# Kernel optimization log

Hardware: AMD Instinct MI355X
Metric: run time of the kernel (lower is better)

The kernel has to match this reference:

```python
import jax, jax.numpy as jnp
import numpy as np

TOP_K = 2  # standard top-2 MoE gating


def setup_inputs() -> dict:
    key = jax.random.key(0)
    k1, k2, k3, k4 = jax.random.split(key, 4)
    T, D, E = 8192, 1024, 8
    x = jax.random.normal(k1, (T, D), dtype=jnp.float32)
    Wg = jax.random.normal(k2, (D, E), dtype=jnp.float32) * (1.0 / np.sqrt(D))
    We = jax.random.normal(k3, (E, D, D), dtype=jnp.float32) * (1.0 / np.sqrt(D))
    be = jax.random.normal(k4, (E, D), dtype=jnp.float32) * 0.02
    return {"x": x, "Wg": Wg, "We": We, "be": be}


def reference(x, Wg, We, be):
    # x: [T, D]; Wg: [D, E]; We: [E, D, D]; be: [E, D]
    T = x.shape[0]
    logits = x @ Wg                          # [T, E]
    probs = jax.nn.softmax(logits, axis=-1)  # [T, E]
    top_v, top_i = jax.lax.top_k(probs, TOP_K)           # [T, K]
    top_v = top_v / jnp.sum(top_v, axis=-1, keepdims=True)
    # dense combine weights [T, E] (zero for non-selected experts)
    cw = jnp.zeros_like(probs).at[jnp.arange(T)[:, None], top_i].add(top_v)
    # per-expert GEMM over all tokens (E is small), then masked combine
    h = jnp.einsum('td,edf->etf', x, We) + be[:, None, :]  # [E, T, D]
    h = jax.nn.relu(h)
    y = jnp.einsum('te,etf->tf', cw, h)                    # [T, D]
    return y
```

## Files before the change

### kernel.cpp

```cpp
#include <hip/hip_runtime.h>

#define T_TOKENS 8192
#define DMODEL   1024
#define NEXP     8

#define BM 128
#define BN 128
#define BK 32
#define NSTEP (DMODEL / BK)

typedef float f32x4  __attribute__((ext_vector_type(4)));
typedef short short8 __attribute__((ext_vector_type(8)));

__device__ __forceinline__ unsigned short f32_to_bf16(float f) {
    unsigned int u = __builtin_bit_cast(unsigned int, f);
    unsigned int r = 0x7FFFu + ((u >> 16) & 1u);
    return (unsigned short)((u + r) >> 16);
}

__global__ __launch_bounds__(256)
void prep(const float* __restrict__ x, const float* __restrict__ Wg,
          const float* __restrict__ We,
          unsigned short* __restrict__ xb, unsigned short* __restrict__ wt,
          int* __restrict__ top_e, float* __restrict__ top_w) {
    __shared__ unsigned short tile[64][72];
    const int bid = blockIdx.x;

    if (bid < 2048) {
        const int wave = threadIdx.x >> 6;
        const int lane = threadIdx.x & 63;
        const int t = bid * 4 + wave;

        float lg[8];
        #pragma unroll
        for (int e = 0; e < 8; ++e) lg[e] = 0.0f;

        const float* xr = x + (size_t)t * DMODEL;
        unsigned short* xo = xb + (size_t)t * DMODEL;

        #pragma unroll
        for (int j = 0; j < 4; ++j) {
            const int d = j * 256 + lane * 4;
            float4 xv = *reinterpret_cast<const float4*>(xr + d);
            ushort4 o;
            o.x = f32_to_bf16(xv.x);
            o.y = f32_to_bf16(xv.y);
            o.z = f32_to_bf16(xv.z);
            o.w = f32_to_bf16(xv.w);
            *reinterpret_cast<ushort4*>(xo + d) = o;
            const float xs[4] = {xv.x, xv.y, xv.z, xv.w};
            #pragma unroll
            for (int c = 0; c < 4; ++c) {
                const float4 wlo = *reinterpret_cast<const float4*>(Wg + (size_t)(d + c) * 8);
                const float4 whi = *reinterpret_cast<const float4*>(Wg + (size_t)(d + c) * 8 + 4);
                lg[0] += xs[c] * wlo.x;  lg[1] += xs[c] * wlo.y;
                lg[2] += xs[c] * wlo.z;  lg[3] += xs[c] * wlo.w;
                lg[4] += xs[c] * whi.x;  lg[5] += xs[c] * whi.y;
                lg[6] += xs[c] * whi.z;  lg[7] += xs[c] * whi.w;
            }
        }
        #pragma unroll
        for (int off = 1; off < 64; off <<= 1) {
            #pragma unroll
            for (int e = 0; e < 8; ++e) lg[e] += __shfl_xor(lg[e], off);
        }

        if (lane == 0) {
            int i1 = 0; float v1 = lg[0];
            #pragma unroll
            for (int e = 1; e < 8; ++e) if (lg[e] > v1) { v1 = lg[e]; i1 = e; }
            int i2 = -1; float v2 = -1e30f;
            #pragma unroll
            for (int e = 0; e < 8; ++e) if (e != i1 && lg[e] > v2) { v2 = lg[e]; i2 = e; }
            const float w1 = 1.0f / (1.0f + __expf(v2 - v1));
            top_e[t] = i1 | (i2 << 4);
            top_w[t] = w1;
        }
    } else {
        const int idx = bid - 2048;
        const int e   = idx >> 8;
        const int rem = idx & 255;
        const int d0  = (rem >> 4) * 64;
        const int f0  = (rem & 15) * 64;
        const float* src = We + ((size_t)e * DMODEL + d0) * DMODEL + f0;
        #pragma unroll
        for (int i = 0; i < 16; ++i) {
            int ix = i * 256 + threadIdx.x;
            int dl = ix >> 6, fl = ix & 63;
            tile[fl][dl] = f32_to_bf16(src[(size_t)dl * DMODEL + fl]);
        }
        __syncthreads();
        unsigned short* dst = wt + ((size_t)e * DMODEL + f0) * DMODEL + d0;
        #pragma unroll
        for (int i = 0; i < 16; ++i) {
            int ix = i * 256 + threadIdx.x;
            int fl = ix >> 6, dl = ix & 63;
            dst[(size_t)fl * DMODEL + dl] = tile[fl][dl];
        }
    }
}

__global__ __launch_bounds__(256)
void compact(const int* __restrict__ top_e, const float* __restrict__ top_w,
             int* __restrict__ counts, int* __restrict__ toks,
             float* __restrict__ wgts, int* __restrict__ rows) {
    const int e    = blockIdx.x;
    const int c    = blockIdx.y;
    const int tid  = threadIdx.x;
    const int wave = tid >> 6;
    const int lane = tid & 63;

    __shared__ int sm[256];
    __shared__ int red[4];
    __shared__ int ws[4];

    int mc = 0;
    const int4* tp = reinterpret_cast<const int4*>(top_e) + tid * 8;
    #pragma unroll
    for (int i = 0; i < 8; ++i) {
        int4 v = tp[i];
        mc += (((v.x & 15) == e) || (((v.x >> 4) & 15) == e)) ? 1 : 0;
        mc += (((v.y & 15) == e) || (((v.y >> 4) & 15) == e)) ? 1 : 0;
        mc += (((v.z & 15) == e) || (((v.z >> 4) & 15) == e)) ? 1 : 0;
        mc += (((v.w & 15) == e) || (((v.w >> 4) & 15) == e)) ? 1 : 0;
    }
    sm[tid] = mc;
    __syncthreads();

    int v = (tid < c * 8) ? sm[tid] : 0;
    #pragma unroll
    for (int off = 1; off < 64; off <<= 1) v += __shfl_xor(v, off);
    if (lane == 0) red[wave] = v;
    __syncthreads();
    const int base = red[0] + red[1] + red[2] + red[3];

    const int t  = c * 256 + tid;
    const int te = top_e[t];
    const int e1 = te & 15;
    const int e2 = (te >> 4) & 15;
    const bool m = (e1 == e) || (e2 == e);
    const unsigned long long b = __ballot(m);
    const int pos_in_wave = __popcll(b & ((1ull << lane) - 1ull));
    if (lane == 0) ws[wave] = __popcll(b);
    __syncthreads();

    int woff = base;
    #pragma unroll
    for (int i = 0; i < 4; ++i) if (i < wave) woff += ws[i];

    if (m) {
        const int pos = woff + pos_in_wave;
        const float w1 = top_w[t];
        toks[e * T_TOKENS + pos] = t;
        wgts[e * T_TOKENS + pos] = (e1 == e) ? w1 : 1.0f - w1;
        rows[t * 2 + ((e1 == e) ? 0 : 1)] = e * T_TOKENS + pos;
    }
    if (c == 31 && tid == 0)
        counts[e] = base + ws[0] + ws[1] + ws[2] + ws[3];
}

__global__ __launch_bounds__(256)
void expert_gemm(const unsigned short* __restrict__ xb,
                 const unsigned short* __restrict__ wt,
                 const float* __restrict__ be,
                 const int* __restrict__ counts,
                 const int* __restrict__ toks,
                 const float* __restrict__ wgts,
                 unsigned short* __restrict__ hpart) {
    const int flat = blockIdx.x + 64 * (blockIdx.y + 8 * blockIdx.z);
    const int fy   = flat & 7;
    const int rest = flat >> 3;
    const int tx   = rest & 63;
    const int e    = rest >> 6;

    const int cnt = counts[e];
    const int p0  = tx * BM;
    if (p0 >= cnt) return;
    const int f0  = fy * BN;

    __shared__ unsigned short lds_w[2][BN * BK];
    __shared__ unsigned short lds_x[2][BM * BK];
    __shared__ int   tok_s[BM];
    __shared__ float wgt_s[BM];

    const int tid  = threadIdx.x;
    const int wave = tid >> 6;
    const int lane = tid & 63;

    if (tid < BM) {
        int p = p0 + tid;
        if (p < cnt) {
            tok_s[tid] = toks[e * T_TOKENS + p];
            wgt_s[tid] = wgts[e * T_TOKENS + p];
        } else {
            tok_s[tid] = 0;
            wgt_s[tid] = 0.0f;
        }
    }
    __syncthreads();

    const char* wsrc[2];
    const char* xsrc[2];
    #pragma unroll
    for (int s = 0; s < 2; ++s) {
        const int q    = wave * 2 + s;
        const int row  = q * 16 + (lane >> 2);
        const int scol = ((lane & 3) << 4) ^ ((row & 3) << 4);
        wsrc[s] = (const char*)wt + ((size_t)(e * DMODEL + f0 + row) * DMODEL) * 2 + scol;
        xsrc[s] = (const char*)xb + ((size_t)tok_s[row] * DMODEL) * 2 + scol;
    }

    auto stage = [&](int buf, int step) {
        const size_t ko = (size_t)step * (BK * 2);
        #pragma unroll
        for (int s = 0; s < 2; ++s) {
            __builtin_amdgcn_global_load_lds(
                (const __attribute__((address_space(1))) void*)(wsrc[s] + ko),
                (__attribute__((address_space(3))) void*)((char*)lds_w[buf] + (wave * 2 + s) * 1024),
                16, 0, 0);
            __builtin_amdgcn_global_load_lds(
                (const __attribute__((address_space(1))) void*)(xsrc[s] + ko),
                (__attribute__((address_space(3))) void*)((char*)lds_x[buf] + (wave * 2 + s) * 1024),
                16, 0, 0);
        }
    };

    f32x4 acc[4][4] = {};

    const int wf = (wave & 1) * 64;
    const int wp = (wave >> 1) * 64;

    auto compute = [&](int buf) {
        short8 afr[4], bfr[4];
        #pragma unroll
        for (int mi = 0; mi < 4; ++mi) {
            const int row = wf + mi * 16 + (lane & 15);
            const int kb  = ((lane >> 4) << 4) ^ ((row & 3) << 4);
            afr[mi] = *(const short8*)((const char*)lds_w[buf] + row * 64 + kb);
        }
        #pragma unroll
        for (int ni = 0; ni < 4; ++ni) {
            const int row = wp + ni * 16 + (lane & 15);
            const int kb  = ((lane >> 4) << 4) ^ ((row & 3) << 4);
            bfr[ni] = *(const short8*)((const char*)lds_x[buf] + row * 64 + kb);
        }
        #pragma unroll
        for (int mi = 0; mi < 4; ++mi)
            #pragma unroll
            for (int ni = 0; ni < 4; ++ni)
                asm("v_mfma_f32_16x16x32_bf16 %0, %1, %2, %0"
                    : "+v"(acc[mi][ni])
                    : "v"(afr[mi]), "v"(bfr[ni]));
    };

    stage(0, 0);
    stage(1, 1);

    #pragma unroll 1
    for (int t = 0; t < NSTEP - 1; ++t) {
        asm volatile("s_waitcnt vmcnt(4)" ::: "memory");
        asm volatile("s_barrier" ::: "memory");
        compute(t & 1);
        asm volatile("s_barrier" ::: "memory");
        if (t + 2 < NSTEP) stage(t & 1, t + 2);
    }
    asm volatile("s_waitcnt vmcnt(0)" ::: "memory");
    asm volatile("s_barrier" ::: "memory");
    compute((NSTEP - 1) & 1);

    #pragma unroll
    for (int ni = 0; ni < 4; ++ni) {
        const int pl = wp + ni * 16 + (lane & 15);
        const int p  = p0 + pl;
        if (p >= cnt) continue;
        const float w = wgt_s[pl];
        unsigned short* hr = hpart + (size_t)(e * T_TOKENS + p) * DMODEL + f0 + wf;
        #pragma unroll
        for (int mi = 0; mi < 4; ++mi) {
            const int fb = mi * 16 + ((lane >> 4) << 2);
            const float* ber = be + (size_t)e * DMODEL + f0 + wf + fb;
            ushort4 o;
            float v0 = acc[mi][ni][0] + ber[0]; v0 = v0 > 0.f ? v0 : 0.f;
            float v1 = acc[mi][ni][1] + ber[1]; v1 = v1 > 0.f ? v1 : 0.f;
            float v2 = acc[mi][ni][2] + ber[2]; v2 = v2 > 0.f ? v2 : 0.f;
            float v3 = acc[mi][ni][3] + ber[3]; v3 = v3 > 0.f ? v3 : 0.f;
            o.x = f32_to_bf16(v0 * w);
            o.y = f32_to_bf16(v1 * w);
            o.z = f32_to_bf16(v2 * w);
            o.w = f32_to_bf16(v3 * w);
            *reinterpret_cast<ushort4*>(hr + fb) = o;
        }
    }
}

__global__ __launch_bounds__(256)
void combine(const unsigned short* __restrict__ hpart,
             const int* __restrict__ rows,
             float* __restrict__ y) {
    const int t = blockIdx.x;
    const int r0 = rows[t * 2 + 0];
    const int r1 = rows[t * 2 + 1];
    const int f = threadIdx.x * 4;
    ushort4 a = *reinterpret_cast<const ushort4*>(hpart + (size_t)r0 * DMODEL + f);
    ushort4 b = *reinterpret_cast<const ushort4*>(hpart + (size_t)r1 * DMODEL + f);
    float4 o;
    o.x = __builtin_bit_cast(float, (unsigned)a.x << 16) + __builtin_bit_cast(float, (unsigned)b.x << 16);
    o.y = __builtin_bit_cast(float, (unsigned)a.y << 16) + __builtin_bit_cast(float, (unsigned)b.y << 16);
    o.z = __builtin_bit_cast(float, (unsigned)a.z << 16) + __builtin_bit_cast(float, (unsigned)b.z << 16);
    o.w = __builtin_bit_cast(float, (unsigned)a.w << 16) + __builtin_bit_cast(float, (unsigned)b.w << 16);
    *reinterpret_cast<float4*>(y + (size_t)t * DMODEL + f) = o;
}

extern "C" void kernel_launch(void* const* d_in, const int* in_sizes, int n_in,
                              void* d_out, int out_size, void* d_ws, size_t ws_size,
                              hipStream_t stream) {
    (void)in_sizes; (void)n_in; (void)out_size; (void)ws_size;
    const float* x  = (const float*)d_in[0];
    const float* Wg = (const float*)d_in[1];
    const float* We = (const float*)d_in[2];
    const float* be = (const float*)d_in[3];
    float* y = (float*)d_out;

    char* ws = (char*)d_ws;
    unsigned short* xb     = (unsigned short*)(ws);
    unsigned short* wt     = (unsigned short*)(ws + (16u << 20));
    size_t off = (32u << 20);
    int*   counts = (int*)(ws + off);    off += 1024;
    int*   toks   = (int*)(ws + off);    off += (size_t)NEXP * T_TOKENS * 4;
    float* wgts   = (float*)(ws + off);  off += (size_t)NEXP * T_TOKENS * 4;
    int*   rows   = (int*)(ws + off);    off += (size_t)T_TOKENS * 2 * 4;
    int*   top_e  = (int*)(ws + off);    off += (size_t)T_TOKENS * 4;
    float* top_w  = (float*)(ws + off);
    unsigned short* hpart = (unsigned short*)(ws + (34u << 20));

    prep<<<dim3(4096), 256, 0, stream>>>(x, Wg, We, xb, wt, top_e, top_w);
    compact<<<dim3(NEXP, 32), 256, 0, stream>>>(top_e, top_w, counts, toks, wgts, rows);
    expert_gemm<<<dim3(T_TOKENS / BM, DMODEL / BN, NEXP), 256, 0, stream>>>(
        xb, wt, be, counts, toks, wgts, hpart);
    combine<<<dim3(T_TOKENS), 256, 0, stream>>>(hpart, rows, y);
}
```

Measured before the change: 122.6 us.

## Use single-buffered BK=64 GEMM loop and vectorize weight transpose in prep

```diff
diff --git a/kernel.cpp b/kernel.cpp
--- a/kernel.cpp
+++ b/kernel.cpp
@@ -6,7 +6,7 @@
 
 #define BM 128
 #define BN 128
-#define BK 32
+#define BK 64
 #define NSTEP (DMODEL / BK)
 
 typedef float f32x4  __attribute__((ext_vector_type(4)));
@@ -84,18 +84,25 @@
         const int f0  = (rem & 15) * 64;
         const float* src = We + ((size_t)e * DMODEL + d0) * DMODEL + f0;
         #pragma unroll
-        for (int i = 0; i < 16; ++i) {
-            int ix = i * 256 + threadIdx.x;
-            int dl = ix >> 6, fl = ix & 63;
-            tile[fl][dl] = f32_to_bf16(src[(size_t)dl * DMODEL + fl]);
+        for (int j = 0; j < 4; ++j) {
+            const int ix = j * 256 + threadIdx.x;
+            const int dl = ix >> 4;
+            const int fq = ix & 15;
+            float4 v = *reinterpret_cast<const float4*>(src + (size_t)dl * DMODEL + fq * 4);
+            tile[fq * 4 + 0][dl] = f32_to_bf16(v.x);
+            tile[fq * 4 + 1][dl] = f32_to_bf16(v.y);
+            tile[fq * 4 + 2][dl] = f32_to_bf16(v.z);
+            tile[fq * 4 + 3][dl] = f32_to_bf16(v.w);
         }
         __syncthreads();
         unsigned short* dst = wt + ((size_t)e * DMODEL + f0) * DMODEL + d0;
         #pragma unroll
-        for (int i = 0; i < 16; ++i) {
-            int ix = i * 256 + threadIdx.x;
-            int fl = ix >> 6, dl = ix & 63;
-            dst[(size_t)fl * DMODEL + dl] = tile[fl][dl];
+        for (int j = 0; j < 4; ++j) {
+            const int ix = j * 256 + threadIdx.x;
+            const int fl = ix >> 4;
+            const int dq = ix & 15;
+            ushort4 v = *reinterpret_cast<const ushort4*>(&tile[fl][dq * 4]);
+            *reinterpret_cast<ushort4*>(dst + (size_t)fl * DMODEL + dq * 4) = v;
         }
     }
 }
@@ -178,8 +185,8 @@
     if (p0 >= cnt) return;
     const int f0  = fy * BN;
 
-    __shared__ unsigned short lds_w[2][BN * BK];
-    __shared__ unsigned short lds_x[2][BM * BK];
+    __shared__ unsigned short lds_w[BN * BK];
+    __shared__ unsigned short lds_x[BM * BK];
     __shared__ int   tok_s[BM];
     __shared__ float wgt_s[BM];
 
@@ -199,74 +206,63 @@
     }
     __syncthreads();
 
-    const char* wsrc[2];
-    const char* xsrc[2];
-    #pragma unroll
-    for (int s = 0; s < 2; ++s) {
-        const int q    = wave * 2 + s;
-        const int row  = q * 16 + (lane >> 2);
-        const int scol = ((lane & 3) << 4) ^ ((row & 3) << 4);
+    const char* wsrc[4];
+    const char* xsrc[4];
+    #pragma unroll
+    for (int s = 0; s < 4; ++s) {
+        const int q    = wave * 4 + s;
+        const int row  = q * 8 + (lane >> 3);
+        const int scol = ((lane & 7) << 4) ^ ((row & 7) << 4);
         wsrc[s] = (const char*)wt + ((size_t)(e * DMODEL + f0 + row) * DMODEL) * 2 + scol;
         xsrc[s] = (const char*)xb + ((size_t)tok_s[row] * DMODEL) * 2 + scol;
     }
 
-    auto stage = [&](int buf, int step) {
-        const size_t ko = (size_t)step * (BK * 2);
-        #pragma unroll
-        for (int s = 0; s < 2; ++s) {
+    f32x4 acc[4][4] = {};
+
+    const int wf = (wave & 1) * 64;
+    const int wp = (wave >> 1) * 64;
+
+    #pragma unroll 1
+    for (int t = 0; t < NSTEP; ++t) {
+        const size_t ko = (size_t)t * BK * 2;
+        #pragma unroll
+        for (int s = 0; s < 4; ++s) {
             __builtin_amdgcn_global_load_lds(
                 (const __attribute__((address_space(1))) void*)(wsrc[s] + ko),
-                (__attribute__((address_space(3))) void*)((char*)lds_w[buf] + (wave * 2 + s) * 1024),
+                (__attribute__((address_space(3))) void*)((char*)lds_w + (wave * 4 + s) * 1024),
                 16, 0, 0);
             __builtin_amdgcn_global_load_lds(
                 (const __attribute__((address_space(1))) void*)(xsrc[s] + ko),
-                (__attribute__((address_space(3))) void*)((char*)lds_x[buf] + (wave * 2 + s) * 1024),
+                (__attribute__((address_space(3))) void*)((char*)lds_x + (wave * 4 + s) * 1024),
                 16, 0, 0);
         }
-    };
-
-    f32x4 acc[4][4] = {};
-
-    const int wf = (wave & 1) * 64;
-    const int wp = (wave >> 1) * 64;
-
-    auto compute = [&](int buf) {
-        short8 afr[4], bfr[4];
-        #pragma unroll
-        for (int mi = 0; mi < 4; ++mi) {
-            const int row = wf + mi * 16 + (lane & 15);
-            const int kb  = ((lane >> 4) << 4) ^ ((row & 3) << 4);
-            afr[mi] = *(const short8*)((const char*)lds_w[buf] + row * 64 + kb);
-        }
-        #pragma unroll
-        for (int ni = 0; ni < 4; ++ni) {
-            const int row = wp + ni * 16 + (lane & 15);
-            const int kb  = ((lane >> 4) << 4) ^ ((row & 3) << 4);
-            bfr[ni] = *(const short8*)((const char*)lds_x[buf] + row * 64 + kb);
-        }
-        #pragma unroll
-        for (int mi = 0; mi < 4; ++mi)
-            #pragma unroll
-            for (int ni = 0; ni < 4; ++ni)
-                asm("v_mfma_f32_16x16x32_bf16 %0, %1, %2, %0"
-                    : "+v"(acc[mi][ni])
-                    : "v"(afr[mi]), "v"(bfr[ni]));
-    };
-
-    stage(0, 0);
-    stage(1, 1);
-
-    #pragma unroll 1
-    for (int t = 0; t < NSTEP - 1; ++t) {
-        asm volatile("s_waitcnt vmcnt(4)" ::: "memory");
-        asm volatile("s_barrier" ::: "memory");
-        compute(t & 1);
-        asm volatile("s_barrier" ::: "memory");
-        if (t + 2 < NSTEP) stage(t & 1, t + 2);
-    }
-    asm volatile("s_waitcnt vmcnt(0)" ::: "memory");
-    asm volatile("s_barrier" ::: "memory");
-    compute((NSTEP - 1) & 1);
+        __syncthreads();
+
+        #pragma unroll
+        for (int kk = 0; kk < 2; ++kk) {
+            short8 afr[4], bfr[4];
+            #pragma unroll
+            for (int mi = 0; mi < 4; ++mi) {
+                const int row = wf + mi * 16 + (lane & 15);
+                const int kb  = (kk * 64 + ((lane >> 4) << 4)) ^ ((row & 7) << 4);
+                afr[mi] = *(const short8*)((const char*)lds_w + row * 128 + kb);
+            }
+            #pragma unroll
+            for (int ni = 0; ni < 4; ++ni) {
+                const int row = wp + ni * 16 + (lane & 15);
+                const int kb  = (kk * 64 + ((lane >> 4) << 4)) ^ ((row & 7) << 4);
+                bfr[ni] = *(const short8*)((const char*)lds_x + row * 128 + kb);
+            }
+            #pragma unroll
+            for (int mi = 0; mi < 4; ++mi)
+                #pragma unroll
+                for (int ni = 0; ni < 4; ++ni)
+                    asm("v_mfma_f32_16x16x32_bf16 %0, %1, %2, %0"
+                        : "+v"(acc[mi][ni])
+                        : "v"(afr[mi]), "v"(bfr[ni]));
+        }
+        __syncthreads();
+    }
 
     #pragma unroll
     for (int ni = 0; ni < 4; ++ni) {
```

Result: faster. 113.4 us (-7.5%).
